# Kernel optimization log

Measured on AMD Instinct MI355X. Metric: run time of the kernel, lower is better.

The kernel has to match this reference:

```python
import jax, jax.numpy as jnp
import numpy as np

B, T, C, H = 2, 4096, 512, 8
D = C // H          # head_size = 64
FF = 4 * C          # 2048
EPS = 1e-5


def _layernorm(x, g, b):
    mu = jnp.mean(x, axis=-1, keepdims=True)
    var = jnp.mean(jnp.square(x - mu), axis=-1, keepdims=True)
    return (x - mu) * jax.lax.rsqrt(var + EPS) * g + b


def setup_inputs() -> dict:
    key = jax.random.key(0)
    ks = jax.random.split(key, 10)
    s = 0.02
    return {
        "x":  jax.random.normal(ks[0], (B, T, C), dtype=jnp.float32),
        # per-head K/Q/V linears (bias=False) packed as [C, C] = concat over heads
        "Wq": jax.random.normal(ks[1], (C, C), dtype=jnp.float32) * s,
        "Wk": jax.random.normal(ks[2], (C, C), dtype=jnp.float32) * s,
        "Wv": jax.random.normal(ks[3], (C, C), dtype=jnp.float32) * s,
        "Wo": jax.random.normal(ks[4], (C, C), dtype=jnp.float32) * s,
        "bo": jnp.zeros((C,), dtype=jnp.float32),
        "W1": jax.random.normal(ks[5], (C, FF), dtype=jnp.float32) * s,
        "b1": jnp.zeros((FF,), dtype=jnp.float32),
        "W2": jax.random.normal(ks[6], (FF, C), dtype=jnp.float32) * s,
        "b2": jnp.zeros((C,), dtype=jnp.float32),
        "g1": jnp.ones((C,), dtype=jnp.float32),
        "be1": jnp.zeros((C,), dtype=jnp.float32),
        "g2": jnp.ones((C,), dtype=jnp.float32),
        "be2": jnp.zeros((C,), dtype=jnp.float32),
    }


def reference(x, Wq, Wk, Wv, Wo, bo, W1, b1, W2, b2, g1, be1, g2, be2):
    # --- self-attention on ln1(x), residual add ---
    h = _layernorm(x, g1, be1)                              # [B,T,C]
    q = (h @ Wq).reshape(B, T, H, D)
    k = (h @ Wk).reshape(B, T, H, D)
    v = (h @ Wv).reshape(B, T, H, D)
    # NOTE: original scales by C**-0.5 (n_embd), NOT head_size**-0.5
    scores = jnp.einsum("bthd,bshd->bhts", q, k) * (C ** -0.5)  # [B,H,T,T]
    causal = jnp.tril(jnp.ones((T, T), dtype=bool))
    scores = jnp.where(causal, scores, -jnp.inf)
    wei = jax.nn.softmax(scores, axis=-1)                   # dropout = identity (eval)
    attn = jnp.einsum("bhts,bshd->bthd", wei, v).reshape(B, T, C)
    x = x + (attn @ Wo + bo)                                # proj dropout = identity
    # --- feed-forward on ln2(x), residual add ---
    h2 = _layernorm(x, g2, be2)
    ff = jax.nn.relu(h2 @ W1 + b1) @ W2 + b2                # dropout = identity
    return x + ff
```

## Files before the change

### kernel.cpp

```cpp
#include <hip/hip_runtime.h>

typedef __attribute__((ext_vector_type(8))) __bf16 bf16x8;
typedef __attribute__((ext_vector_type(4))) __bf16 bf16x4;
typedef __attribute__((ext_vector_type(4))) float f32x4;
typedef __attribute__((ext_vector_type(4))) unsigned int u32x4;
typedef __attribute__((ext_vector_type(4))) unsigned short u16x4;
typedef __attribute__((ext_vector_type(8))) unsigned short u16x8;
typedef __attribute__((ext_vector_type(4))) short s16x4;
typedef unsigned short u16;

static __device__ __forceinline__ u16 f2b(float f) {
    unsigned u = __builtin_bit_cast(unsigned, f);
    u = (u + 0x7FFFu + ((u >> 16) & 1u)) >> 16;
    return (u16)u;
}
static __device__ __forceinline__ float b2f(u16 u) {
    return __builtin_bit_cast(float, ((unsigned)u) << 16);
}
static __device__ __forceinline__ float fexp2(float x) {
#if __has_builtin(__builtin_amdgcn_exp2f)
    return __builtin_amdgcn_exp2f(x);
#else
    return exp2f(x);
#endif
}
static __device__ __forceinline__ f32x4 mfma16(bf16x4 a, bf16x4 b, f32x4 c) {
#if __has_builtin(__builtin_amdgcn_mfma_f32_16x16x16_bf16)
    return __builtin_amdgcn_mfma_f32_16x16x16_bf16(a, b, c, 0, 0, 0);
#else
    return __builtin_amdgcn_mfma_f32_16x16x16bf16_1k(
        __builtin_bit_cast(s16x4, a), __builtin_bit_cast(s16x4, b), c, 0, 0, 0);
#endif
}

static __device__ __forceinline__ void gload16(const u16* g, u16* l) {
    __builtin_amdgcn_global_load_lds(
        (const __attribute__((address_space(1))) unsigned int*)g,
        (__attribute__((address_space(3))) unsigned int*)l, 16, 0, 0);
}

__global__ __launch_bounds__(256) void prep_w(
    const float* __restrict__ Wq, const float* __restrict__ Wk,
    const float* __restrict__ Wv, const float* __restrict__ Wo,
    const float* __restrict__ W1, const float* __restrict__ W2,
    u16* __restrict__ WqkvT, u16* __restrict__ WoT,
    u16* __restrict__ W1T, u16* __restrict__ W2T)
{
    const int i = blockIdx.x;
    const float* src; u16* dst; int K, N, nt, kt;
    if (i < 1024) {
        const int z = i >> 8, idx = i & 255;
        K = 512; N = 512; nt = (idx & 15) * 32; kt = (idx >> 4) * 32;
        if (z == 0)      { src = Wq; dst = WqkvT; }
        else if (z == 1) { src = Wk; dst = WqkvT + 512*512; }
        else if (z == 2) { src = Wv; dst = WqkvT + 1024*512; }
        else             { src = Wo; dst = WoT; }
    } else if (i < 2048) {
        const int idx = i - 1024;
        src = W1; dst = W1T; K = 512; N = 2048;
        nt = (idx & 63) * 32; kt = (idx >> 6) * 32;
    } else {
        const int idx = i - 2048;
        src = W2; dst = W2T; K = 2048; N = 512;
        nt = (idx & 15) * 32; kt = (idx >> 4) * 32;
    }
    __shared__ float tile[32][33];
    const int tx = threadIdx.x & 31, ty = threadIdx.x >> 5;
    #pragma unroll
    for (int r = 0; r < 4; ++r)
        tile[ty + r*8][tx] = src[(size_t)(kt + ty + r*8) * N + nt + tx];
    __syncthreads();
    #pragma unroll
    for (int r = 0; r < 4; ++r)
        dst[(size_t)(nt + ty + r*8) * K + kt + tx] = f2b(tile[tx][ty + r*8]);
}

__global__ __launch_bounds__(256) void ln_rows(
    const float* __restrict__ x, const float* __restrict__ g,
    const float* __restrict__ b, u16* __restrict__ out)
{
    const int row = blockIdx.x * 4 + (threadIdx.x >> 6);
    const int lane = threadIdx.x & 63;
    const float* xr = x + (size_t)row * 512;
    f32x4 v0 = *(const f32x4*)(xr + lane * 4);
    f32x4 v1 = *(const f32x4*)(xr + 256 + lane * 4);
    float s = v0[0]+v0[1]+v0[2]+v0[3]+v1[0]+v1[1]+v1[2]+v1[3];
    #pragma unroll
    for (int o = 1; o < 64; o <<= 1) s += __shfl_xor(s, o);
    const float mu = s * (1.0f / 512.0f);
    float s2 = 0.f;
    #pragma unroll
    for (int i = 0; i < 4; ++i) { float d0 = v0[i]-mu, d1 = v1[i]-mu; s2 += d0*d0 + d1*d1; }
    #pragma unroll
    for (int o = 1; o < 64; o <<= 1) s2 += __shfl_xor(s2, o);
    const float inv = rsqrtf(s2 * (1.0f/512.0f) + 1e-5f);
    f32x4 g0 = *(const f32x4*)(g + lane*4), g1 = *(const f32x4*)(g + 256 + lane*4);
    f32x4 b0 = *(const f32x4*)(b + lane*4), b1 = *(const f32x4*)(b + 256 + lane*4);
    u16x4 p0, p1;
    #pragma unroll
    for (int i = 0; i < 4; ++i) {
        p0[i] = f2b((v0[i]-mu)*inv*g0[i] + b0[i]);
        p1[i] = f2b((v1[i]-mu)*inv*g1[i] + b1[i]);
    }
    u16* orow = out + (size_t)row * 512;
    *(u16x4*)(orow + lane*4)       = p0;
    *(u16x4*)(orow + 256 + lane*4) = p1;
}

template<int FLAGS, int NB, int GX>
__global__ __launch_bounds__(256) void gemm_bt(
    const u16* __restrict__ A, const u16* __restrict__ BT,
    const int N, const int K,
    const float* __restrict__ bias, const float* __restrict__ res,
    void* __restrict__ outv, u16* __restrict__ vt)
{
    constexpr int RING = (NB == 2) ? 3 : 4;
    __shared__ __attribute__((aligned(16))) u16 As[RING * 4096];
    __shared__ __attribute__((aligned(16))) u16 Bs[RING * 2048 * NB];
    const int fid = blockIdx.x;
    const int xcd = fid & 7, s8 = fid >> 3;
    const int colb = s8 % GX, rl = s8 / GX;
    const int m0 = (xcd*8 + rl) << 7;
    const int n0 = colb * (64 * NB);
    const int tid = threadIdx.x, lane = tid & 63, w = tid >> 6;
    const int wr2 = w >> 1, wc = w & 1;
    const int g = lane >> 4, c = lane & 15;
    const f32x4 fz = {0.f, 0.f, 0.f, 0.f};

    f32x4 acc[4][2 * NB];
    #pragma unroll
    for (int m = 0; m < 4; ++m)
      #pragma unroll
      for (int n = 0; n < 2 * NB; ++n) acc[m][n] = fz;

    const int srow = tid >> 2;
    const int scs = (((tid & 3) ^ (srow & 3)) * 8);
    const u16* Ag = A  + (size_t)(m0 + srow)*K + scs;
    const u16* Bg = BT + (size_t)(n0 + srow)*K + scs;
    const size_t rstep = (size_t)64 * K;

    const int nkt = K >> 5;
    auto stage = [&](int slot, int kt) {
        const int k0 = kt << 5;
        u16* ad = &As[0] + slot*4096 + w*512;
        gload16(Ag + k0,         ad);
        gload16(Ag + rstep + k0, ad + 2048);
        u16* bd = &Bs[0] + slot*2048*NB + w*512;
        gload16(Bg + k0, bd);
        if constexpr (NB == 2) gload16(Bg + rstep + k0, bd + 2048);
    };
    stage(0, 0);
    stage(1, (1 < nkt) ? 1 : 0);
    if constexpr (RING == 4) stage(2, (2 < nkt) ? 2 : 0);

    for (int kt = 0; kt < nkt; ++kt) {
        if constexpr (NB == 2) asm volatile("s_waitcnt vmcnt(4)" ::: "memory");
        else                   asm volatile("s_waitcnt vmcnt(6)" ::: "memory");
        __builtin_amdgcn_s_barrier();
        asm volatile("" ::: "memory");
        {
            int tp = kt + RING - 1; if (tp >= nkt) tp = nkt - 1;
            int sl = kt + RING - 1; sl -= (sl / RING) * RING;
            stage(sl, tp);
        }
        const int rd = kt - (kt / RING) * RING;
        const u16* Ab = &As[0] + rd*4096;
        const u16* Bb = &Bs[0] + rd*2048*NB;
        bf16x8 af[4], bfr[2 * NB];
        #pragma unroll
        for (int m = 0; m < 4; ++m) {
            const int row = wr2*64 + m*16 + c;
            af[m] = *(const bf16x8*)(Ab + row*32 + (((g*16) ^ ((row&3)<<4)) >> 1));
        }
        #pragma unroll
        for (int n = 0; n < 2 * NB; ++n) {
            const int row = wc*(32*NB) + n*16 + c;
            bfr[n] = *(const bf16x8*)(Bb + row*32 + (((g*16) ^ ((row&3)<<4)) >> 1));
        }
        #pragma unroll
        for (int m = 0; m < 4; ++m)
          #pragma unroll
          for (int n = 0; n < 2 * NB; ++n)
            acc[m][n] = __builtin_amdgcn_mfma_f32_16x16x32_bf16(af[m], bfr[n], acc[m][n], 0, 0, 0);
    }

    #pragma unroll
    for (int m = 0; m < 4; ++m) {
        const int row = m0 + wr2*64 + m*16 + 4*g;
        #pragma unroll
        for (int n = 0; n < 2 * NB; ++n) {
            const int col = n0 + wc*(32*NB) + n*16 + c;
            const float bv = (FLAGS & 1) ? bias[col] : 0.0f;
            float vv[4];
            #pragma unroll
            for (int r = 0; r < 4; ++r) {
                float v = acc[m][n][r] + bv;
                if (FLAGS & 16) v *= (col < 512) ? 0.0637587246f : 1.0f;
                if (FLAGS & 2) v += res[(size_t)(row + r)*N + col];
                if (FLAGS & 4) v = fmaxf(v, 0.0f);
                vv[r] = v;
            }
            if ((FLAGS & 32) && col >= 1024) {
                u16x4 pv;
                #pragma unroll
                for (int r = 0; r < 4; ++r) pv[r] = f2b(vv[r]);
                *(u16x4*)(vt + (size_t)((row >> 12)*512 + (col - 1024))*4096
                             + (row & 4095)) = pv;
            } else if (FLAGS & 8) {
                #pragma unroll
                for (int r = 0; r < 4; ++r)
                    ((float*)outv)[(size_t)(row + r)*N + col] = vv[r];
            } else {
                #pragma unroll
                for (int r = 0; r < 4; ++r)
                    ((u16*)outv)[(size_t)(row + r)*N + col] = f2b(vv[r]);
            }
        }
    }
}

__global__ __launch_bounds__(256, 3) void attn_fwd(
    const u16* __restrict__ qkv, const u16* __restrict__ vT,
    u16* __restrict__ part, u16* __restrict__ att)
{
    const int fid = blockIdx.x + 160 * blockIdx.y;
    const int xcd = fid & 7, s0i = fid >> 3;
    const int half = (s0i >= 160) ? 1 : 0;
    const int bh = xcd*2 + half, b = bh >> 3, h = bh & 7;
    const int i = 159 - (s0i - half*160);
    int qt, cch, nch;
    if (i < 16)      { qt = i;                         cch = 0;          nch = 1; }
    else if (i < 48) { int j = i-16; qt = 16 + (j>>1); cch = j & 1;      nch = 2; }
    else if (i < 96) { int j = i-48; int d3 = j/3; qt = 32 + d3; cch = j - 3*d3; nch = 3; }
    else             { int j = i-96; qt = 48 + (j>>2); cch = j & 3;      nch = 4; }
    const int ntl = qt + 1;
    const int t0 = (cch * ntl) / nch;
    const int t1 = ((cch + 1) * ntl) / nch;
    const int single = (nch == 1);

    const int tid = threadIdx.x, lane = tid & 63, w = tid >> 6;
    const int g = lane >> 4, c16 = lane & 15;
    __shared__ __attribute__((aligned(16))) u16 smem[20480];
    u16* Wb = smem + w*5120;
    float* lbuf = (float*)smem + 5120;

    const u16* qp  = qkv + (size_t)b*4096*1536 + h*64;
    const u16* kp  = qp + 512;
    const u16* vtp = vT + (size_t)bh*64*4096;

    const u16* kgA = kp + (size_t)(16*w + (lane>>3))*1536
                        + (((lane&7) ^ ((lane>>3)&7)) * 8);
    const u16* kgB = kgA + (size_t)8*1536;
    const int sd = lane >> 1;
    const u16* vgA = vtp + (size_t)sd*4096 + 16*w + (((lane&1) ^ ((sd>>2)&1)) * 8);
    const u16* vgB = vgA + (size_t)32*4096;

    const int kOff0 = c16*64 + ((g ^ (c16&7)) * 8);
    const int kOff1 = c16*64 + (((4+g) ^ (c16&7)) * 8);
    const int vroff = c16*16 + (((g>>1) ^ ((c16>>2)&1)) * 8) + (g&1)*4;

    const int Q0 = qt*64;
    bf16x8 qB[4][2];
    #pragma unroll
    for (int sub = 0; sub < 4; ++sub) {
        const u16* qr = qp + (size_t)(Q0 + sub*16 + c16)*1536 + g*8;
        qB[sub][0] = *(const bf16x8*)(qr);
        qB[sub][1] = *(const bf16x8*)(qr + 32);
    }

    const f32x4 fz = {0.f,0.f,0.f,0.f};
    f32x4 oacc[4][4];
    #pragma unroll
    for (int dt = 0; dt < 4; ++dt)
      #pragma unroll
      for (int sub = 0; sub < 4; ++sub) oacc[dt][sub] = fz;
    float lsum[4] = {0.f, 0.f, 0.f, 0.f};

    {
        const int kv0 = t0 << 6;
        u16* vd = Wb + 3072 + (t0 & 1)*1024;
        gload16(vgA + kv0, vd); gload16(vgB + kv0, vd + 512);
        u16* kd = Wb + (t0 % 3)*1024;
        const size_t ko0 = (size_t)kv0 * 1536;
        gload16(kgA + ko0, kd); gload16(kgB + ko0, kd + 512);
        const int tp1 = (t0+1 < t1) ? (t0+1) : (t1-1);
        u16* kd1 = Wb + ((t0+1) % 3)*1024;
        const size_t ko1 = (size_t)(tp1 << 6)*1536;
        gload16(kgA + ko1, kd1); gload16(kgB + ko1, kd1 + 512);
    }
    int krd = t0 % 3;
    int kwr = krd + 2; if (kwr >= 3) kwr -= 3;

    for (int t = t0; t < t1; ++t) {
        {
            const int tpv = (t+1 < t1) ? (t+1) : (t1-1);
            u16* vd = Wb + 3072 + ((t+1) & 1)*1024;
            gload16(vgA + (tpv << 6), vd); gload16(vgB + (tpv << 6), vd + 512);
            const int tpk = (t+2 < t1) ? (t+2) : (t1-1);
            u16* kd = Wb + kwr*1024;
            const size_t ko = (size_t)(tpk << 6)*1536;
            gload16(kgA + ko, kd); gload16(kgB + ko, kd + 512);
        }
        asm volatile("s_waitcnt vmcnt(6)" ::: "memory");
        const u16* Kb  = Wb + krd*1024;
        const u16* Vbp = Wb + 3072 + (t & 1)*1024;
        const bf16x8 kc0 = *(const bf16x8*)(Kb + kOff0);
        const bf16x8 kc1 = *(const bf16x8*)(Kb + kOff1);
        bf16x4 va[4];
        #pragma unroll
        for (int dt = 0; dt < 4; ++dt)
            va[dt] = *(const bf16x4*)(Vbp + dt*256 + vroff);
        f32x4 s[4];
        #pragma unroll
        for (int sub = 0; sub < 4; ++sub) {
            f32x4 sv = __builtin_amdgcn_mfma_f32_16x16x32_bf16(kc0, qB[sub][0], fz, 0, 0, 0);
            s[sub]   = __builtin_amdgcn_mfma_f32_16x16x32_bf16(kc1, qB[sub][1], sv, 0, 0, 0);
        }
        bf16x4 pt[4];
        if (t < qt) {
            #pragma unroll
            for (int sub = 0; sub < 4; ++sub) {
                float p0 = fexp2(s[sub][0]), p1 = fexp2(s[sub][1]);
                float p2 = fexp2(s[sub][2]), p3 = fexp2(s[sub][3]);
                lsum[sub] += (p0 + p1) + (p2 + p3);
                bf16x4 pv;
                pv[0] = (__bf16)p0; pv[1] = (__bf16)p1;
                pv[2] = (__bf16)p2; pv[3] = (__bf16)p3;
                pt[sub] = pv;
            }
        } else {
            const int kvbase = t*64 + 16*w + 4*g;
            #pragma unroll
            for (int sub = 0; sub < 4; ++sub) {
                const int qi = Q0 + sub*16 + c16;
                bf16x4 pv; float a = 0.f;
                #pragma unroll
                for (int r = 0; r < 4; ++r) {
                    float p = (kvbase + r <= qi) ? fexp2(s[sub][r]) : 0.0f;
                    a += p; pv[r] = (__bf16)p;
                }
                lsum[sub] += a; pt[sub] = pv;
            }
        }
        #pragma unroll
        for (int dt = 0; dt < 4; ++dt)
          #pragma unroll
          for (int sub = 0; sub < 4; ++sub)
            oacc[dt][sub] = mfma16(va[dt], pt[sub], oacc[dt][sub]);
        krd = (krd == 2) ? 0 : krd + 1;
        kwr = (kwr == 2) ? 0 : kwr + 1;
    }

    #pragma unroll
    for (int sub = 0; sub < 4; ++sub) {
        float v = lsum[sub];
        v += __shfl_xor(v, 16);
        v += __shfl_xor(v, 32);
        lsum[sub] = v;
    }

    asm volatile("s_waitcnt vmcnt(0)" ::: "memory");
    __syncthreads();
    #pragma unroll
    for (int sub = 0; sub < 4; ++sub)
        if (g == 0) lbuf[w*64 + sub*16 + c16] = lsum[sub];

    float* img = (float*)smem;
    f32x4 ofin[4];
    float ltot[4];
    #pragma unroll
    for (int dt = 0; dt < 4; ++dt) {
        #pragma unroll
        for (int sub = 0; sub < 4; ++sub)
            *(f32x4*)(img + w*1280 + (sub*16 + c16)*20 + g*4) = oacc[dt][sub];
        __syncthreads();
        if (dt == 0) {
            #pragma unroll
            for (int sub = 0; sub < 4; ++sub) {
                const int qr = sub*16 + c16;
                ltot[sub] = lbuf[qr] + lbuf[64 + qr] + lbuf[128 + qr] + lbuf[192 + qr];
            }
        }
        if (w == dt) {
            #pragma unroll
            for (int sub = 0; sub < 4; ++sub) {
                const int off = (sub*16 + c16)*20 + g*4;
                f32x4 a0 = *(const f32x4*)(img + off);
                f32x4 a1 = *(const f32x4*)(img + 1280 + off);
                f32x4 a2 = *(const f32x4*)(img + 2560 + off);
                f32x4 a3 = *(const f32x4*)(img + 3840 + off);
                ofin[sub] = (a0 + a1) + (a2 + a3);
            }
        }
        __syncthreads();
    }

    const int dbase = 16*w + 4*g;
    if (single) {
        #pragma unroll
        for (int sub = 0; sub < 4; ++sub) {
            const int qrow = sub*16 + c16;
            const float inv = 1.0f / ltot[sub];
            const f32x4 o = ofin[sub];
            u16x4 ov;
            ov[0] = f2b(o[0]*inv); ov[1] = f2b(o[1]*inv);
            ov[2] = f2b(o[2]*inv); ov[3] = f2b(o[3]*inv);
            *(u16x4*)(att + (size_t)(b*4096 + Q0 + qrow)*512 + h*64 + dbase) = ov;
        }
    } else {
        u16* onum = part + (size_t)(bh*160 + i) * 4224;
        float* lout = (float*)(onum + 4096);
        #pragma unroll
        for (int sub = 0; sub < 4; ++sub) {
            const int qrow = sub*16 + c16;
            const f32x4 o = ofin[sub];
            u16x4 ov;
            ov[0] = f2b(o[0]); ov[1] = f2b(o[1]);
            ov[2] = f2b(o[2]); ov[3] = f2b(o[3]);
            *(u16x4*)(onum + qrow*64 + dbase) = ov;
            if (w == 0 && g == 0) lout[qrow] = ltot[sub];
        }
    }
}

__global__ __launch_bounds__(256) void attn_merge(
    const u16* __restrict__ part, u16* __restrict__ att)
{
    const int qt = 16 + blockIdx.x, bh = blockIdx.y, b = bh >> 3, h = bh & 7;
    int start, n;
    if (qt < 32)      { start = 16 + 2*(qt-16); n = 2; }
    else if (qt < 48) { start = 48 + 3*(qt-32); n = 3; }
    else              { start = 96 + 4*(qt-48); n = 4; }
    const int t = threadIdx.x;
    const int row = t >> 2, c0 = (t & 3) * 16;
    float acc[16];
    #pragma unroll
    for (int j = 0; j < 16; ++j) acc[j] = 0.f;
    float lt = 0.f;
    const u16* p0 = part + (size_t)(bh*160 + start) * 4224;
    for (int ci = 0; ci < n; ++ci) {
        const u16* pc = p0 + (size_t)ci * 4224;
        lt += ((const float*)(pc + 4096))[row];
        u16x8 a = *(const u16x8*)(pc + row*64 + c0);
        u16x8 bq = *(const u16x8*)(pc + row*64 + c0 + 8);
        #pragma unroll
        for (int j = 0; j < 8; ++j) { acc[j] += b2f(a[j]); acc[8+j] += b2f(bq[j]); }
    }
    const float inv = 1.0f / lt;
    u16x8 o1, o2;
    #pragma unroll
    for (int j = 0; j < 8; ++j) { o1[j] = f2b(acc[j]*inv); o2[j] = f2b(acc[8+j]*inv); }
    u16* dst = att + (size_t)(b*4096 + qt*64 + row)*512 + h*64 + c0;
    *(u16x8*)dst = o1;
    *(u16x8*)(dst + 8) = o2;
}

extern "C" void kernel_launch(void* const* d_in, const int* in_sizes, int n_in,
                              void* d_out, int out_size, void* d_ws, size_t ws_size,
                              hipStream_t stream)
{
    (void)in_sizes; (void)n_in; (void)out_size; (void)ws_size;
    const float* x   = (const float*)d_in[0];
    const float* Wq  = (const float*)d_in[1];
    const float* Wk  = (const float*)d_in[2];
    const float* Wv  = (const float*)d_in[3];
    const float* Wo  = (const float*)d_in[4];
    const float* bo  = (const float*)d_in[5];
    const float* W1  = (const float*)d_in[6];
    const float* b1  = (const float*)d_in[7];
    const float* W2  = (const float*)d_in[8];
    const float* b2  = (const float*)d_in[9];
    const float* g1  = (const float*)d_in[10];
    const float* be1 = (const float*)d_in[11];
    const float* g2  = (const float*)d_in[12];
    const float* be2 = (const float*)d_in[13];

    char* ws = (char*)d_ws;
    u16*   WqkvT = (u16*)(ws + 0);
    u16*   WoT   = (u16*)(ws + 1572864);
    u16*   W1T   = (u16*)(ws + 2097152);
    u16*   W2T   = (u16*)(ws + 4194304);
    u16*   H     = (u16*)(ws + 6291456);
    u16*   PART  = (u16*)(ws + 6291456);
    float* X2    = (float*)(ws + 14680064);
    u16*   QKV   = (u16*)(ws + 31457280);
    u16*   VT    = (u16*)(ws + 56623104);
    u16*   ATT   = (u16*)(ws + 65011712);
    u16*   F1    = (u16*)(ws + 31457280);

    prep_w<<<3072, 256, 0, stream>>>(Wq, Wk, Wv, Wo, W1, W2,
                                     WqkvT, WoT, W1T, W2T);
    ln_rows<<<2048, 256, 0, stream>>>(x, g1, be1, H);
    gemm_bt<48, 2, 12><<<768, 256, 0, stream>>>(H, WqkvT, 1536, 512,
                                                nullptr, nullptr, QKV, VT);
    attn_fwd<<<dim3(160, 16), 256, 0, stream>>>(QKV, VT, PART, ATT);
    attn_merge<<<dim3(48, 16), 256, 0, stream>>>(PART, ATT);
    gemm_bt<11, 1, 8><<<512, 256, 0, stream>>>(ATT, WoT, 512, 512,
                                               bo, x, X2, nullptr);
    ln_rows<<<2048, 256, 0, stream>>>(X2, g2, be2, H);
    gemm_bt<5, 2, 16><<<1024, 256, 0, stream>>>(H, W1T, 2048, 512,
                                                b1, nullptr, F1, nullptr);
    gemm_bt<11, 1, 8><<<512, 256, 0, stream>>>(F1, W2T, 512, 2048,
                                               b2, X2, (float*)d_out, nullptr);
}
```

Measured before the change: 194.4 us.

## Replace GEMM with 64x64 tile kernel using 4-deep LDS ring

Replaces the templated 128xN GEMM with a smaller 64x64 output-tile kernel. Each wave computes a 16x64 strip, and the A and B tiles are staged through a 4-slot LDS ring. All four linear-layer GEMMs now launch 2-4x more blocks. This is meant to raise occupancy and fill all CUs on these modest-size matrices, at the cost of lower arithmetic intensity per block and more global/L2 traffic for re-read operands.

```diff
diff --git a/kernel.cpp b/kernel.cpp
--- a/kernel.cpp
+++ b/kernel.cpp
@@ -107,114 +107,94 @@
     *(u16x4*)(orow + 256 + lane*4) = p1;
 }
 
-template<int FLAGS, int NB, int GX>
-__global__ __launch_bounds__(256) void gemm_bt(
+template<int FLAGS, int GX>
+__global__ __launch_bounds__(256) void gemm_m64(
     const u16* __restrict__ A, const u16* __restrict__ BT,
     const int N, const int K,
     const float* __restrict__ bias, const float* __restrict__ res,
     void* __restrict__ outv, u16* __restrict__ vt)
 {
-    constexpr int RING = (NB == 2) ? 3 : 4;
-    __shared__ __attribute__((aligned(16))) u16 As[RING * 4096];
-    __shared__ __attribute__((aligned(16))) u16 Bs[RING * 2048 * NB];
+    __shared__ __attribute__((aligned(16))) u16 As[4 * 2048];
+    __shared__ __attribute__((aligned(16))) u16 Bs[4 * 2048];
     const int fid = blockIdx.x;
     const int xcd = fid & 7, s8 = fid >> 3;
     const int colb = s8 % GX, rl = s8 / GX;
-    const int m0 = (xcd*8 + rl) << 7;
-    const int n0 = colb * (64 * NB);
+    const int m0 = (xcd*16 + rl) << 6;
+    const int n0 = colb << 6;
     const int tid = threadIdx.x, lane = tid & 63, w = tid >> 6;
-    const int wr2 = w >> 1, wc = w & 1;
     const int g = lane >> 4, c = lane & 15;
     const f32x4 fz = {0.f, 0.f, 0.f, 0.f};
 
-    f32x4 acc[4][2 * NB];
-    #pragma unroll
-    for (int m = 0; m < 4; ++m)
-      #pragma unroll
-      for (int n = 0; n < 2 * NB; ++n) acc[m][n] = fz;
+    f32x4 acc[4] = {fz, fz, fz, fz};
 
     const int srow = tid >> 2;
     const int scs = (((tid & 3) ^ (srow & 3)) * 8);
     const u16* Ag = A  + (size_t)(m0 + srow)*K + scs;
     const u16* Bg = BT + (size_t)(n0 + srow)*K + scs;
-    const size_t rstep = (size_t)64 * K;
 
     const int nkt = K >> 5;
     auto stage = [&](int slot, int kt) {
         const int k0 = kt << 5;
-        u16* ad = &As[0] + slot*4096 + w*512;
-        gload16(Ag + k0,         ad);
-        gload16(Ag + rstep + k0, ad + 2048);
-        u16* bd = &Bs[0] + slot*2048*NB + w*512;
-        gload16(Bg + k0, bd);
-        if constexpr (NB == 2) gload16(Bg + rstep + k0, bd + 2048);
+        gload16(Ag + k0, &As[0] + slot*2048 + w*512);
+        gload16(Bg + k0, &Bs[0] + slot*2048 + w*512);
     };
     stage(0, 0);
     stage(1, (1 < nkt) ? 1 : 0);
-    if constexpr (RING == 4) stage(2, (2 < nkt) ? 2 : 0);
-
+    stage(2, (2 < nkt) ? 2 : 0);
+
+    const int arow = w*16 + c;
+    const int aoff = arow*32 + ((g ^ (arow & 3)) * 8);
     for (int kt = 0; kt < nkt; ++kt) {
-        if constexpr (NB == 2) asm volatile("s_waitcnt vmcnt(4)" ::: "memory");
-        else                   asm volatile("s_waitcnt vmcnt(6)" ::: "memory");
+        asm volatile("s_waitcnt vmcnt(4)" ::: "memory");
         __builtin_amdgcn_s_barrier();
         asm volatile("" ::: "memory");
         {
-            int tp = kt + RING - 1; if (tp >= nkt) tp = nkt - 1;
-            int sl = kt + RING - 1; sl -= (sl / RING) * RING;
-            stage(sl, tp);
-        }
-        const int rd = kt - (kt / RING) * RING;
-        const u16* Ab = &As[0] + rd*4096;
-        const u16* Bb = &Bs[0] + rd*2048*NB;
-        bf16x8 af[4], bfr[2 * NB];
-        #pragma unroll
-        for (int m = 0; m < 4; ++m) {
-            const int row = wr2*64 + m*16 + c;
-            af[m] = *(const bf16x8*)(Ab + row*32 + (((g*16) ^ ((row&3)<<4)) >> 1));
-        }
-        #pragma unroll
-        for (int n = 0; n < 2 * NB; ++n) {
-            const int row = wc*(32*NB) + n*16 + c;
-            bfr[n] = *(const bf16x8*)(Bb + row*32 + (((g*16) ^ ((row&3)<<4)) >> 1));
-        }
-        #pragma unroll
-        for (int m = 0; m < 4; ++m)
-          #pragma unroll
-          for (int n = 0; n < 2 * NB; ++n)
-            acc[m][n] = __builtin_amdgcn_mfma_f32_16x16x32_bf16(af[m], bfr[n], acc[m][n], 0, 0, 0);
-    }
-
-    #pragma unroll
-    for (int m = 0; m < 4; ++m) {
-        const int row = m0 + wr2*64 + m*16 + 4*g;
-        #pragma unroll
-        for (int n = 0; n < 2 * NB; ++n) {
-            const int col = n0 + wc*(32*NB) + n*16 + c;
-            const float bv = (FLAGS & 1) ? bias[col] : 0.0f;
-            float vv[4];
-            #pragma unroll
-            for (int r = 0; r < 4; ++r) {
-                float v = acc[m][n][r] + bv;
-                if (FLAGS & 16) v *= (col < 512) ? 0.0637587246f : 1.0f;
-                if (FLAGS & 2) v += res[(size_t)(row + r)*N + col];
-                if (FLAGS & 4) v = fmaxf(v, 0.0f);
-                vv[r] = v;
-            }
-            if ((FLAGS & 32) && col >= 1024) {
-                u16x4 pv;
-                #pragma unroll
-                for (int r = 0; r < 4; ++r) pv[r] = f2b(vv[r]);
-                *(u16x4*)(vt + (size_t)((row >> 12)*512 + (col - 1024))*4096
-                             + (row & 4095)) = pv;
-            } else if (FLAGS & 8) {
-                #pragma unroll
-                for (int r = 0; r < 4; ++r)
-                    ((float*)outv)[(size_t)(row + r)*N + col] = vv[r];
-            } else {
-                #pragma unroll
-                for (int r = 0; r < 4; ++r)
-                    ((u16*)outv)[(size_t)(row + r)*N + col] = f2b(vv[r]);
-            }
+            int tp = kt + 3; if (tp >= nkt) tp = nkt - 1;
+            stage((kt + 3) & 3, tp);
+        }
+        const int rd = kt & 3;
+        const u16* Ab = &As[0] + rd*2048;
+        const u16* Bb = &Bs[0] + rd*2048;
+        const bf16x8 af = *(const bf16x8*)(Ab + aoff);
+        bf16x8 bfr[4];
+        #pragma unroll
+        for (int n = 0; n < 4; ++n) {
+            const int row = n*16 + c;
+            bfr[n] = *(const bf16x8*)(Bb + row*32 + ((g ^ (row & 3)) * 8));
+        }
+        #pragma unroll
+        for (int n = 0; n < 4; ++n)
+            acc[n] = __builtin_amdgcn_mfma_f32_16x16x32_bf16(af, bfr[n], acc[n], 0, 0, 0);
+    }
+
+    const int row = m0 + w*16 + 4*g;
+    #pragma unroll
+    for (int n = 0; n < 4; ++n) {
+        const int col = n0 + n*16 + c;
+        const float bv = (FLAGS & 1) ? bias[col] : 0.0f;
+        float vv[4];
+        #pragma unroll
+        for (int r = 0; r < 4; ++r) {
+            float v = acc[n][r] + bv;
+            if (FLAGS & 16) v *= (col < 512) ? 0.0637587246f : 1.0f;
+            if (FLAGS & 2) v += res[(size_t)(row + r)*N + col];
+            if (FLAGS & 4) v = fmaxf(v, 0.0f);
+            vv[r] = v;
+        }
+        if ((FLAGS & 32) && col >= 1024) {
+            u16x4 pv;
+            #pragma unroll
+            for (int r = 0; r < 4; ++r) pv[r] = f2b(vv[r]);
+            *(u16x4*)(vt + (size_t)((row >> 12)*512 + (col - 1024))*4096
+                         + (row & 4095)) = pv;
+        } else if (FLAGS & 8) {
+            #pragma unroll
+            for (int r = 0; r < 4; ++r)
+                ((float*)outv)[(size_t)(row + r)*N + col] = vv[r];
+        } else {
+            #pragma unroll
+            for (int r = 0; r < 4; ++r)
+                ((u16*)outv)[(size_t)(row + r)*N + col] = f2b(vv[r]);
         }
     }
 }
@@ -491,15 +471,15 @@
     prep_w<<<3072, 256, 0, stream>>>(Wq, Wk, Wv, Wo, W1, W2,
                                      WqkvT, WoT, W1T, W2T);
     ln_rows<<<2048, 256, 0, stream>>>(x, g1, be1, H);
-    gemm_bt<48, 2, 12><<<768, 256, 0, stream>>>(H, WqkvT, 1536, 512,
-                                                nullptr, nullptr, QKV, VT);
+    gemm_m64<48, 24><<<3072, 256, 0, stream>>>(H, WqkvT, 1536, 512,
+                                               nullptr, nullptr, QKV, VT);
     attn_fwd<<<dim3(160, 16), 256, 0, stream>>>(QKV, VT, PART, ATT);
     attn_merge<<<dim3(48, 16), 256, 0, stream>>>(PART, ATT);
-    gemm_bt<11, 1, 8><<<512, 256, 0, stream>>>(ATT, WoT, 512, 512,
-                                               bo, x, X2, nullptr);
+    gemm_m64<11, 8><<<1024, 256, 0, stream>>>(ATT, WoT, 512, 512,
+                                              bo, x, X2, nullptr);
     ln_rows<<<2048, 256, 0, stream>>>(X2, g2, be2, H);
-    gemm_bt<5, 2, 16><<<1024, 256, 0, stream>>>(H, W1T, 2048, 512,
-                                                b1, nullptr, F1, nullptr);
-    gemm_bt<11, 1, 8><<<512, 256, 0, stream>>>(F1, W2T, 512, 2048,
-                                               b2, X2, (float*)d_out, nullptr);
-}
+    gemm_m64<5, 32><<<4096, 256, 0, stream>>>(H, W1T, 2048, 512,
+                                              b1, nullptr, F1, nullptr);
+    gemm_m64<11, 8><<<1024, 256, 0, stream>>>(F1, W2T, 512, 2048,
+                                              b2, X2, (float*)d_out, nullptr);
+}
```

After: 207.0 us. 6.5% more time.
